# Performance work log

Measured on AMD Instinct MI355X. Metric: run time of the kernel, lower is better.

Reference implementation:

```python
import jax, jax.numpy as jnp
import numpy as np

N1, N2, P, D = 8, 8, 1024, 768  # 8 query / 8 normal images, 32x32 patches, ViT-B dim
PH = PW = 32
H = W = 512


def setup_inputs() -> dict:
    key = jax.random.key(0)
    k1, k2 = jax.random.split(key)
    feats = jax.random.normal(k1, (N1, P, D), dtype=jnp.float32)
    nfeats = jax.random.normal(k2, (N2, P, D), dtype=jnp.float32)
    return {"feats": feats, "nfeats": nfeats, "ph": PH, "pw": PW, "h": H, "w": W}


def _bilinear_resize(x, out_h, out_w):
    # x: [N, h, w] -> [N, out_h, out_w]; matches F.interpolate(mode='bilinear', align_corners=False)
    n, h, w = x.shape
    sy = (jnp.arange(out_h, dtype=x.dtype) + 0.5) * (h / out_h) - 0.5
    sx = (jnp.arange(out_w, dtype=x.dtype) + 0.5) * (w / out_w) - 0.5
    y0f = jnp.floor(sy)
    x0f = jnp.floor(sx)
    wy = (sy - y0f)[None, :, None]  # [1, out_h, 1]
    wx = (sx - x0f)[None, None, :]  # [1, 1, out_w]
    y0 = jnp.clip(y0f.astype(jnp.int32), 0, h - 1)
    y1 = jnp.clip(y0f.astype(jnp.int32) + 1, 0, h - 1)
    x0 = jnp.clip(x0f.astype(jnp.int32), 0, w - 1)
    x1 = jnp.clip(x0f.astype(jnp.int32) + 1, 0, w - 1)
    v00 = x[:, y0[:, None], x0[None, :]]
    v01 = x[:, y0[:, None], x1[None, :]]
    v10 = x[:, y1[:, None], x0[None, :]]
    v11 = x[:, y1[:, None], x1[None, :]]
    top = v00 * (1 - wx) + v01 * wx
    bot = v10 * (1 - wx) + v11 * wx
    return top * (1 - wy) + bot * wy


def reference(feats, nfeats, ph, pw, h, w):
    # L2-normalize patch embeddings (as in forward: f / f.norm(dim=-1, keepdim=True))
    f = feats / jnp.linalg.norm(feats, axis=-1, keepdims=True)   # [N1, P, D]
    g = nfeats / jnp.linalg.norm(nfeats, axis=-1, keepdims=True)  # [N2, P, D]
    n1 = f.shape[0]
    # cdist(feats.reshape(N1*P,D), nfeats.reshape(N2*P,D)).reshape(N1,P,N2,P).permute(0,2,1,3)
    gram = jnp.einsum('npd,mqd->nmpq', f, g)                      # [N1, N2, P, P]
    fa2 = jnp.sum(f * f, axis=-1)                                 # [N1, P]
    gb2 = jnp.sum(g * g, axis=-1)                                 # [N2, P]
    d2 = fa2[:, None, :, None] + gb2[None, :, None, :] - 2.0 * gram
    dist = jnp.sqrt(jnp.maximum(d2, 0.0)) * 0.5                   # distances / 2
    # nearest-normal-patch distance per query patch (bg mask is all ones here)
    scores_patch = jnp.min(dist, axis=-1)                         # [N1, N2, P]
    scores = jnp.mean(jnp.max(scores_patch, axis=-1), axis=1)     # [N1]
    sp = jnp.mean(scores_patch, axis=1).reshape(n1, ph, pw)       # [N1, PH, PW]
    scores_pixel = _bilinear_resize(sp, h, w)                     # [N1, H, W]
    return scores, scores_pixel
```

## Files before the change

kernel.cpp:

```cpp
#include <hip/hip_runtime.h>
#include <hip/hip_bf16.h>
#include <stdint.h>

#define N1 8
#define N2 8
#define PP 1024
#define DD 768
#define PH 32
#define PW 32
#define OH 512
#define OW 512

#define NKT 12

typedef int i32x4 __attribute__((ext_vector_type(4)));

__global__ __launch_bounds__(256) void nrm_kernel(
    const float* __restrict__ inA, const float* __restrict__ inB,
    char* __restrict__ outA, char* __restrict__ outB) {
  int row = blockIdx.x;
  const float* src;
  char* dst;
  if (row < N1 * PP) {
    src = inA + (size_t)row * DD;
    dst = outA + (size_t)row * DD;
  } else {
    row -= N1 * PP;
    src = inB + (size_t)row * DD;
    dst = outB + (size_t)row * DD;
  }
  const int t = threadIdx.x;
  const float v0 = src[t], v1 = src[t + 256], v2 = src[t + 512];
  float s = v0 * v0 + v1 * v1 + v2 * v2;
#pragma unroll
  for (int m = 32; m; m >>= 1) s += __shfl_xor(s, m, 64);
  __shared__ float red[4];
  const int wave = t >> 6, lane = t & 63;
  if (lane == 0) red[wave] = s;
  __syncthreads();
  const float inv = 127.0f / sqrtf(red[0] + red[1] + red[2] + red[3]);
  dst[t]       = (char)__float2int_rn(v0 * inv);
  dst[t + 256] = (char)__float2int_rn(v1 * inv);
  dst[t + 512] = (char)__float2int_rn(v2 * inv);
}

__device__ __forceinline__ void gll16(const char* src, char* dst) {
  __builtin_amdgcn_global_load_lds(
      (const __attribute__((address_space(1))) void*)src,
      (__attribute__((address_space(3))) void*)dst, 16, 0, 0);
}

__global__ __launch_bounds__(512, 2) void grami8_kernel(
    const char* __restrict__ fq, const char* __restrict__ gq,
    int* __restrict__ rowmaxI) {
  __shared__ __align__(16) char lds[4][4][8192];

  const int bid = blockIdx.x;
  const int wg = (bid & 7) * 128 + (bid >> 3);
  const int pair = wg >> 4;
  const int tile = wg & 15;
  const int fn = pair >> 3, gm = pair & 7;
  const int mt = tile >> 2, nt = tile & 3;
  const int brow = mt * 256, bcol = nt * 256;

  const int t = threadIdx.x;
  const int lane = t & 63, wave = t >> 6;
  const int lr = lane & 15, lk = lane >> 4;
  const int wr = wave >> 2, wc = wave & 3;

  const char* rowA = fq + ((size_t)fn * PP + brow) * DD;
  const char* rowB = gq + ((size_t)gm * PP + bcol) * DD;

  const int xs = (t * 16) ^ (((t >> 3) & 7) << 4);
  const int srow = xs >> 6;
  const int scol = xs & 63;

  const int swzv = ((lr >> 1) & 7) << 4;
  const int abase = (lr * 64 + lk * 16) ^ swzv;
  const int bbase = (wc & 1) * 4096 + ((lr * 64 + lk * 16) ^ swzv);

#define STAGE(rowPtr, h, kt, slotptr)                                     \
  gll16(rowPtr + (size_t)((h) * 128 + srow) * DD + (kt) * 64 + scol,      \
        (slotptr) + t * 16)

  i32x4 acc[8][4];
#pragma unroll
  for (int i = 0; i < 8; ++i)
#pragma unroll
    for (int j = 0; j < 4; ++j) acc[i][j] = (i32x4){0, 0, 0, 0};

#pragma unroll
  for (int kk = 0; kk < 3; ++kk) {
    STAGE(rowB, 0, kk, &lds[kk][2][0]);
    STAGE(rowB, 1, kk, &lds[kk][3][0]);
    STAGE(rowA, 0, kk, &lds[kk][0][0]);
    STAGE(rowA, 1, kk, &lds[kk][1][0]);
  }
  asm volatile("s_waitcnt vmcnt(8)" ::: "memory");
  __builtin_amdgcn_s_barrier();
  asm volatile("" ::: "memory");

#pragma unroll 1
  for (int k = 0; k < NKT; ++k) {
    const char* Ab = &lds[k & 3][wr][0];
    const char* Bb = &lds[k & 3][2 + (wc >> 1)][0];

    i32x4 a[8], b[4];
#pragma unroll
    for (int m = 0; m < 8; ++m)
      a[m] = *(const i32x4*)(Ab + abase + m * 1024);
#pragma unroll
    for (int n = 0; n < 4; ++n)
      b[n] = *(const i32x4*)(Bb + bbase + n * 1024);

    if (k + 3 < NKT) {
      const int ss = (k + 3) & 3;
      STAGE(rowB, 0, k + 3, &lds[ss][2][0]);
      STAGE(rowB, 1, k + 3, &lds[ss][3][0]);
      STAGE(rowA, 0, k + 3, &lds[ss][0][0]);
      STAGE(rowA, 1, k + 3, &lds[ss][1][0]);
    }

#pragma unroll
    for (int m = 0; m < 8; ++m)
#pragma unroll
      for (int n = 0; n < 4; ++n)
        acc[m][n] = __builtin_amdgcn_mfma_i32_16x16x64_i8(a[m], b[n],
                                                          acc[m][n], 0, 0, 0);

    if (k < NKT - 3) {
      asm volatile("s_waitcnt vmcnt(8)" ::: "memory");
    } else if (k == NKT - 3) {
      asm volatile("s_waitcnt vmcnt(4)" ::: "memory");
    } else if (k == NKT - 2) {
      asm volatile("s_waitcnt vmcnt(0)" ::: "memory");
    }
    __builtin_amdgcn_s_barrier();
    asm volatile("" ::: "memory");
  }

  int* rm = rowmaxI + (size_t)(fn * 8 + gm) * PP;
#pragma unroll
  for (int m = 0; m < 8; ++m) {
#pragma unroll
    for (int r = 0; r < 4; ++r) {
      int vv = max(max(acc[m][0][r], acc[m][1][r]),
                   max(acc[m][2][r], acc[m][3][r]));
      vv = max(vv, __shfl_xor(vv, 1, 64));
      vv = max(vv, __shfl_xor(vv, 2, 64));
      vv = max(vv, __shfl_xor(vv, 4, 64));
      vv = max(vv, __shfl_xor(vv, 8, 64));
      if (lr == 0) {
        const int row = brow + wr * 128 + m * 16 + lk * 4 + r;
        atomicMax(&rm[row], vv);
      }
    }
  }
#undef STAGE
}

__global__ __launch_bounds__(256) void finalize_kernel(
    const int* __restrict__ rowmaxI, float* __restrict__ sp,
    float* __restrict__ scores) {
  const int n = blockIdx.x, t = threadIdx.x;
  const int lane = t & 63, wave = t >> 6;
  __shared__ float red[4];
  __shared__ float maxd[N2];
  float spacc[4] = {0.f, 0.f, 0.f, 0.f};
  for (int m = 0; m < N2; ++m) {
    float lmax = -1e30f;
#pragma unroll
    for (int i = 0; i < 4; ++i) {
      const int p = t + i * 256;
      const float g = (float)rowmaxI[(size_t)(n * N2 + m) * PP + p] *
                      (1.0f / 16129.0f);
      const float d = 0.5f * sqrtf(fmaxf(0.f, 2.f - 2.f * g));
      spacc[i] += d;
      lmax = fmaxf(lmax, d);
    }
#pragma unroll
    for (int msk = 32; msk; msk >>= 1) lmax = fmaxf(lmax, __shfl_xor(lmax, msk, 64));
    if (lane == 0) red[wave] = lmax;
    __syncthreads();
    if (t == 0) maxd[m] = fmaxf(fmaxf(red[0], red[1]), fmaxf(red[2], red[3]));
    __syncthreads();
  }
  if (t == 0) {
    float s = 0.f;
    for (int m = 0; m < N2; ++m) s += maxd[m];
    scores[n] = s * (1.0f / N2);
  }
#pragma unroll
  for (int i = 0; i < 4; ++i)
    sp[(size_t)n * PP + t + i * 256] = spacc[i] * (1.0f / N2);
}

__global__ __launch_bounds__(256) void resize_kernel(
    const float* __restrict__ sp, float* __restrict__ out) {
  const int idx = blockIdx.x * 256 + threadIdx.x;
  const int ox = idx & (OW - 1);
  const int oy = (idx >> 9) & (OH - 1);
  const int n = idx >> 18;
  const float sy = (oy + 0.5f) * ((float)PH / OH) - 0.5f;
  const float sx = (ox + 0.5f) * ((float)PW / OW) - 0.5f;
  const float y0f = floorf(sy), x0f = floorf(sx);
  const float wy = sy - y0f, wx = sx - x0f;
  int y0 = (int)y0f, x0 = (int)x0f;
  int y1 = y0 + 1, x1 = x0 + 1;
  y0 = min(max(y0, 0), PH - 1);
  y1 = min(max(y1, 0), PH - 1);
  x0 = min(max(x0, 0), PW - 1);
  x1 = min(max(x1, 0), PW - 1);
  const float* s = sp + (size_t)n * PP;
  const float v00 = s[y0 * PW + x0], v01 = s[y0 * PW + x1];
  const float v10 = s[y1 * PW + x0], v11 = s[y1 * PW + x1];
  const float top = v00 * (1.f - wx) + v01 * wx;
  const float bot = v10 * (1.f - wx) + v11 * wx;
  out[idx] = top * (1.f - wy) + bot * wy;
}

extern "C" void kernel_launch(void* const* d_in, const int* in_sizes, int n_in,
                              void* d_out, int out_size, void* d_ws, size_t ws_size,
                              hipStream_t stream) {
  const float* feats = (const float*)d_in[0];
  const float* nfeats = (const float*)d_in[1];
  float* out = (float*)d_out;

  char* ws = (char*)d_ws;
  const size_t FQ_BYTES = (size_t)N1 * PP * DD;
  char* fq = ws;
  char* gq = ws + FQ_BYTES;
  int* rowmaxI = (int*)(ws + 2 * FQ_BYTES);
  float* sp = (float*)(ws + 2 * FQ_BYTES + (size_t)N1 * N2 * PP * 4);

  hipMemsetAsync(rowmaxI, 0x80, (size_t)N1 * N2 * PP * 4, stream);

  nrm_kernel<<<(N1 + N2) * PP, 256, 0, stream>>>(feats, nfeats, fq, gq);

  grami8_kernel<<<1024, 512, 0, stream>>>(fq, gq, rowmaxI);

  finalize_kernel<<<N1, 256, 0, stream>>>(rowmaxI, sp, out);
  resize_kernel<<<(N1 * OH * OW) / 256, 256, 0, stream>>>(sp, out + 8);
}
```

Before: 121.2 us.

## Use 128-wide K tiles with double buffering in int8 gram kernel

Restructures the int8 MFMA gram GEMM to stage 128-byte K slices per iteration (6 iterations instead of 12) in a 2-slot double buffer, replacing the 4-slot 3-deep prefetch ring. The LDS layout and XOR swizzle change to 128-byte rows, and each iteration runs two MFMA sub-steps. The aim is to halve the barrier and waitcnt overhead per K step and issue larger loads. In exchange, prefetch depth drops to one stage and every iteration waits on vmcnt(0), which may expose global load latency.

```diff
diff --git a/kernel.cpp b/kernel.cpp
--- a/kernel.cpp
+++ b/kernel.cpp
@@ -11,7 +11,7 @@
 #define OH 512
 #define OW 512
 
-#define NKT 12
+#define NKT 6
 
 typedef int i32x4 __attribute__((ext_vector_type(4)));
 
@@ -53,7 +53,7 @@
 __global__ __launch_bounds__(512, 2) void grami8_kernel(
     const char* __restrict__ fq, const char* __restrict__ gq,
     int* __restrict__ rowmaxI) {
-  __shared__ __align__(16) char lds[4][4][8192];
+  __shared__ __align__(16) char lds[2][2][32768];
 
   const int bid = blockIdx.x;
   const int wg = (bid & 7) * 128 + (bid >> 3);
@@ -71,17 +71,28 @@
   const char* rowA = fq + ((size_t)fn * PP + brow) * DD;
   const char* rowB = gq + ((size_t)gm * PP + bcol) * DD;
 
-  const int xs = (t * 16) ^ (((t >> 3) & 7) << 4);
-  const int srow = xs >> 6;
-  const int scol = xs & 63;
-
-  const int swzv = ((lr >> 1) & 7) << 4;
-  const int abase = (lr * 64 + lk * 16) ^ swzv;
-  const int bbase = (wc & 1) * 4096 + ((lr * 64 + lk * 16) ^ swzv);
-
-#define STAGE(rowPtr, h, kt, slotptr)                                     \
-  gll16(rowPtr + (size_t)((h) * 128 + srow) * DD + (kt) * 64 + scol,      \
-        (slotptr) + t * 16)
+  int srow[4], scol[4];
+#pragma unroll
+  for (int j = 0; j < 4; ++j) {
+    const int c = t + j * 512;
+    const int x = (c * 16) ^ (((c >> 3) & 7) << 4);
+    srow[j] = x >> 7;
+    scol[j] = x & 127;
+  }
+
+  const int swzm = (lr & 7) << 4;
+  const int fk0 = (0 * 64 + lk * 16) ^ swzm;
+  const int fk1 = (1 * 64 + lk * 16) ^ swzm;
+  const int abase = (wr * 128 + lr) * 128;
+  const int bbase = (wc * 64 + lr) * 128;
+
+#define STAGE(rowPtr, kt, slot, mat)                                       \
+  do {                                                                     \
+    _Pragma("unroll")                                                      \
+    for (int j = 0; j < 4; ++j)                                            \
+      gll16(rowPtr + (size_t)srow[j] * DD + (kt) * 128 + scol[j],          \
+            &lds[slot][mat][(t + j * 512) * 16]);                          \
+  } while (0)
 
   i32x4 acc[8][4];
 #pragma unroll
@@ -89,52 +100,50 @@
 #pragma unroll
     for (int j = 0; j < 4; ++j) acc[i][j] = (i32x4){0, 0, 0, 0};
 
-#pragma unroll
-  for (int kk = 0; kk < 3; ++kk) {
-    STAGE(rowB, 0, kk, &lds[kk][2][0]);
-    STAGE(rowB, 1, kk, &lds[kk][3][0]);
-    STAGE(rowA, 0, kk, &lds[kk][0][0]);
-    STAGE(rowA, 1, kk, &lds[kk][1][0]);
-  }
-  asm volatile("s_waitcnt vmcnt(8)" ::: "memory");
+  STAGE(rowB, 0, 0, 1);
+  STAGE(rowA, 0, 0, 0);
+  asm volatile("s_waitcnt vmcnt(0)" ::: "memory");
   __builtin_amdgcn_s_barrier();
   asm volatile("" ::: "memory");
 
 #pragma unroll 1
   for (int k = 0; k < NKT; ++k) {
-    const char* Ab = &lds[k & 3][wr][0];
-    const char* Bb = &lds[k & 3][2 + (wc >> 1)][0];
+    const char* Ab = &lds[k & 1][0][0];
+    const char* Bb = &lds[k & 1][1][0];
+
+    if (k + 1 < NKT) {
+      const int ns = (k + 1) & 1;
+      STAGE(rowB, k + 1, ns, 1);
+      STAGE(rowA, k + 1, ns, 0);
+    }
 
     i32x4 a[8], b[4];
 #pragma unroll
     for (int m = 0; m < 8; ++m)
-      a[m] = *(const i32x4*)(Ab + abase + m * 1024);
+      a[m] = *(const i32x4*)(Ab + abase + m * 2048 + fk0);
 #pragma unroll
     for (int n = 0; n < 4; ++n)
-      b[n] = *(const i32x4*)(Bb + bbase + n * 1024);
-
-    if (k + 3 < NKT) {
-      const int ss = (k + 3) & 3;
-      STAGE(rowB, 0, k + 3, &lds[ss][2][0]);
-      STAGE(rowB, 1, k + 3, &lds[ss][3][0]);
-      STAGE(rowA, 0, k + 3, &lds[ss][0][0]);
-      STAGE(rowA, 1, k + 3, &lds[ss][1][0]);
-    }
-
+      b[n] = *(const i32x4*)(Bb + bbase + n * 2048 + fk0);
 #pragma unroll
     for (int m = 0; m < 8; ++m)
 #pragma unroll
       for (int n = 0; n < 4; ++n)
         acc[m][n] = __builtin_amdgcn_mfma_i32_16x16x64_i8(a[m], b[n],
                                                           acc[m][n], 0, 0, 0);
-
-    if (k < NKT - 3) {
-      asm volatile("s_waitcnt vmcnt(8)" ::: "memory");
-    } else if (k == NKT - 3) {
-      asm volatile("s_waitcnt vmcnt(4)" ::: "memory");
-    } else if (k == NKT - 2) {
-      asm volatile("s_waitcnt vmcnt(0)" ::: "memory");
-    }
+#pragma unroll
+    for (int m = 0; m < 8; ++m)
+      a[m] = *(const i32x4*)(Ab + abase + m * 2048 + fk1);
+#pragma unroll
+    for (int n = 0; n < 4; ++n)
+      b[n] = *(const i32x4*)(Bb + bbase + n * 2048 + fk1);
+#pragma unroll
+    for (int m = 0; m < 8; ++m)
+#pragma unroll
+      for (int n = 0; n < 4; ++n)
+        acc[m][n] = __builtin_amdgcn_mfma_i32_16x16x64_i8(a[m], b[n],
+                                                          acc[m][n], 0, 0, 0);
+
+    asm volatile("s_waitcnt vmcnt(0)" ::: "memory");
     __builtin_amdgcn_s_barrier();
     asm volatile("" ::: "memory");
   }
```

After: 116.0 us. 4.3% less time.
